# Optimization experiments

Measured on AMD Instinct MI355X. Metric: run time of the kernel, lower is better.

Reference implementation:

```python
import jax, jax.numpy as jnp
import numpy as np
import math

B, N, L = 1, 256, 384
D_MSA, D_PAIR, H, DH = 256, 128, 8, 32


def layer_norm(x, g, b, eps=1e-5):
    m = jnp.mean(x, axis=-1, keepdims=True)
    v = jnp.var(x, axis=-1, keepdims=True)
    return (x - m) * jax.lax.rsqrt(v + eps) * g + b


def setup_inputs() -> dict:
    key = jax.random.key(0)
    ks = jax.random.split(key, 16)
    hd = H * DH
    w = lambda k, shp, s=0.05: (jax.random.normal(k, shp, dtype=jnp.float32) * s)
    return {
        "msa": jax.random.normal(ks[0], (B, N, L, D_MSA), dtype=jnp.float32),
        "pair": jax.random.normal(ks[1], (B, L, L, D_PAIR), dtype=jnp.float32),
        "ln_msa_g": jnp.ones((D_MSA,), jnp.float32),
        "ln_msa_b": jnp.zeros((D_MSA,), jnp.float32),
        "ln_pair_g": jnp.ones((D_PAIR,), jnp.float32),
        "ln_pair_b": jnp.zeros((D_PAIR,), jnp.float32),
        "sw_q_w": w(ks[2], (D_MSA, hd)),
        "sw_q_b": jnp.zeros((hd,), jnp.float32),
        "sw_k_w": w(ks[3], (D_MSA, hd)),
        "sw_k_b": jnp.zeros((hd,), jnp.float32),
        "wq": w(ks[4], (D_MSA, hd)),
        "wk": w(ks[5], (D_MSA, hd)),
        "wv": w(ks[6], (D_MSA, hd)),
        "wb": w(ks[7], (D_PAIR, H)),
        "wg": w(ks[8], (D_MSA, hd)),
        "bg": jnp.ones((hd,), jnp.float32),
        "wo": w(ks[9], (hd, D_MSA)),
        "bo": jnp.zeros((D_MSA,), jnp.float32),
    }


def reference(msa, pair, ln_msa_g, ln_msa_b, ln_pair_g, ln_pair_b,
              sw_q_w, sw_q_b, sw_k_w, sw_k_b,
              wq, wk, wv, wb, wg, bg, wo, bo):
    b, n, l, _ = msa.shape
    scale = 1.0 / math.sqrt(DH)

    msa_n = layer_norm(msa, ln_msa_g, ln_msa_b)
    pair_n = layer_norm(pair, ln_pair_g, ln_pair_b)

    # SequenceWeight: attention of target seq (row 0) over all N rows, per (L, head)
    tar = msa_n[:, 0]                                       # [B,L,D]
    swq = (tar @ sw_q_w + sw_q_b).reshape(b, l, H, DH) * scale
    swk = (msa_n @ sw_k_w + sw_k_b).reshape(b, n, l, H, DH)
    sw_logits = jnp.einsum('blhd,bnlhd->bnlh', swq, swk)    # [B,N,L,H]
    seq_weight = jax.nn.softmax(sw_logits, axis=1)          # softmax over N (dropout: eval)

    query = (msa_n @ wq).reshape(b, n, l, H, DH) * seq_weight[..., None]
    key = (msa_n @ wk).reshape(b, n, l, H, DH) * scale
    value = (msa_n @ wv).reshape(b, n, l, H, DH)
    bias = pair_n @ wb                                      # [B,L,L,H]
    gate = jax.nn.sigmoid(msa_n @ wg + bg)                  # [B,N,L,H*DH]

    attn = jnp.einsum('bsqhd,bskhd->bqkh', query, key) + bias
    attn = jax.nn.softmax(attn, axis=-2)                    # over k axis
    out = jnp.einsum('bqkh,bskhd->bsqhd', attn, value).reshape(b, n, l, H * DH)
    out = gate * out
    return out @ wo + bo
```

## Files before the change

### kernel.cpp

```cpp
#include <hip/hip_runtime.h>
#include <stdint.h>

#define NSEQ 256
#define LSEQ 384
#define DM   256
#define DP   128
#define NH   8
#define DHD  32
#define NL   (NSEQ*LSEQ)
#define LL   (LSEQ*LSEQ)
#define SCALE 0.17677669529663687f

typedef unsigned short u16;
typedef short bf16x8 __attribute__((ext_vector_type(8)));
typedef float f32x4 __attribute__((ext_vector_type(4)));

__device__ __forceinline__ float b2f(u16 s){
  union { uint32_t u; float f; } v; v.u = ((uint32_t)s)<<16; return v.f;
}
__device__ __forceinline__ u16 f2b(float f){
  union { float f; uint32_t u; } v; v.f = f;
  uint32_t u = v.u;
  return (u16)((u + 0x7FFFu + ((u>>16)&1u)) >> 16);
}
__device__ __forceinline__ float wsum(float x){
  #pragma unroll
  for(int o=32;o>0;o>>=1) x += __shfl_xor(x,o,64);
  return x;
}
__device__ __forceinline__ float wmax(float x){
  #pragma unroll
  for(int o=32;o>0;o>>=1) x = fmaxf(x, __shfl_xor(x,o,64));
  return x;
}
__device__ __forceinline__ void gload16(const void* g, void* l){
  __builtin_amdgcn_global_load_lds((const __attribute__((address_space(1))) void*)g,
      (__attribute__((address_space(3))) void*)l, 16, 0, 0);
}

__global__ __launch_bounds__(256) void k_ln_msa(const float* __restrict__ msa,
    const float* __restrict__ g, const float* __restrict__ b, u16* __restrict__ out){
  int lane = threadIdx.x & 63;
  int64_t row = (int64_t)blockIdx.x*4 + (threadIdx.x>>6);
  const float4 x = *(const float4*)(msa + row*DM + lane*4);
  float s = x.x+x.y+x.z+x.w;
  float q = x.x*x.x+x.y*x.y+x.z*x.z+x.w*x.w;
  s = wsum(s); q = wsum(q);
  float mean = s*(1.0f/DM);
  float rstd = rsqrtf(q*(1.0f/DM) - mean*mean + 1e-5f);
  int c = lane*4;
  float4 gv = *(const float4*)(g+c);
  float4 bv = *(const float4*)(b+c);
  ushort4 o;
  o.x=f2b((x.x-mean)*rstd*gv.x+bv.x);
  o.y=f2b((x.y-mean)*rstd*gv.y+bv.y);
  o.z=f2b((x.z-mean)*rstd*gv.z+bv.z);
  o.w=f2b((x.w-mean)*rstd*gv.w+bv.w);
  *(ushort4*)(out + row*DM + c) = o;
}

__global__ __launch_bounds__(256) void k_wconv(const float* __restrict__ wq,
    const float* __restrict__ wk, const float* __restrict__ wv,
    const float* __restrict__ wg, const float* __restrict__ wo,
    u16* __restrict__ WTall, u16* __restrict__ WOT){
  __shared__ float tile[64][65];
  int z = blockIdx.z;
  const float* src = (z==0)?wq:(z==1)?wk:(z==2)?wv:(z==3)?wg:wo;
  u16* dst = (z<4) ? (WTall + z*DM*DM) : WOT;
  int k0 = blockIdx.x*64, n0 = blockIdx.y*64, t = threadIdx.x;
  int r = t>>4, c4 = (t&15)*4;
  #pragma unroll
  for(int it=0; it<4; it++){
    float4 v = *(const float4*)(src + (int64_t)(k0 + it*16 + r)*DM + n0 + c4);
    tile[it*16+r][c4+0]=v.x; tile[it*16+r][c4+1]=v.y;
    tile[it*16+r][c4+2]=v.z; tile[it*16+r][c4+3]=v.w;
  }
  __syncthreads();
  #pragma unroll
  for(int it=0; it<4; it++){
    int nl = it*16 + r, kl = c4;
    ushort4 o;
    o.x=f2b(tile[kl+0][nl]); o.y=f2b(tile[kl+1][nl]);
    o.z=f2b(tile[kl+2][nl]); o.w=f2b(tile[kl+3][nl]);
    *(ushort4*)(dst + (int64_t)(n0+nl)*DM + k0 + kl) = o;
  }
}

__global__ __launch_bounds__(256) void k_u(const u16* __restrict__ msa_n,
    const float* __restrict__ sw_q_w, const float* __restrict__ sw_q_b,
    const float* __restrict__ sw_k_w, float* __restrict__ u){
  __shared__ float tar[DM];
  __shared__ float swq[DM];
  int l = blockIdx.x, t = threadIdx.x;
  tar[t] = b2f(msa_n[(int64_t)l*DM + t]);
  __syncthreads();
  float acc = sw_q_b[t];
  for(int c=0;c<DM;c++) acc += tar[c]*sw_q_w[c*DM + t];
  swq[t] = acc * SCALE;
  __syncthreads();
  float res[NH];
  #pragma unroll
  for(int h=0;h<NH;h++){
    float a = 0.f;
    #pragma unroll
    for(int d=0;d<DHD;d+=4){
      float4 w = *(const float4*)(sw_k_w + t*DM + h*DHD + d);
      a += w.x*swq[h*DHD+d] + w.y*swq[h*DHD+d+1] + w.z*swq[h*DHD+d+2] + w.w*swq[h*DHD+d+3];
    }
    res[h]=a;
  }
  #pragma unroll
  for(int h=0;h<NH;h++) u[((int64_t)l*NH + h)*DM + t] = res[h];
}

__global__ __launch_bounds__(256) void k_seqw(const u16* __restrict__ msa_n,
    const float* __restrict__ u, float* __restrict__ sw){
  __shared__ float ul[NH*DM];
  __shared__ float lg[NH*256];
  __shared__ float mx[NH], sm[NH];
  int l = blockIdx.x, t = threadIdx.x;
  #pragma unroll
  for(int h=0;h<NH;h++) ul[h*DM+t] = u[((int64_t)l*NH+h)*DM + t];
  __syncthreads();
  float acc[NH] = {};
  const u16* row = msa_n + ((int64_t)t*LSEQ + l)*DM;
  for(int c=0;c<DM;c+=4){
    ushort4 xv = *(const ushort4*)(row + c);
    float x0=b2f(xv.x), x1=b2f(xv.y), x2=b2f(xv.z), x3=b2f(xv.w);
    #pragma unroll
    for(int h=0;h<NH;h++)
      acc[h] += x0*ul[h*DM+c] + x1*ul[h*DM+c+1] + x2*ul[h*DM+c+2] + x3*ul[h*DM+c+3];
  }
  #pragma unroll
  for(int h=0;h<NH;h++) lg[h*256+t] = acc[h];
  __syncthreads();
  int wv = t>>6, ln = t&63;
  for(int h=wv; h<NH; h+=4){
    float a=lg[h*256+ln], b=lg[h*256+ln+64], c=lg[h*256+ln+128], d=lg[h*256+ln+192];
    float m = wmax(fmaxf(fmaxf(a,b),fmaxf(c,d)));
    float e = __expf(a-m)+__expf(b-m)+__expf(c-m)+__expf(d-m);
    e = wsum(e);
    if(ln==0){ mx[h]=m; sm[h]=1.f/e; }
  }
  __syncthreads();
  float o[NH];
  #pragma unroll
  for(int h=0;h<NH;h++) o[h] = __expf(acc[h]-mx[h])*sm[h];
  float* dst = sw + ((int64_t)t*LSEQ + l)*NH;
  *(float4*)dst     = make_float4(o[0],o[1],o[2],o[3]);
  *(float4*)(dst+4) = make_float4(o[4],o[5],o[6],o[7]);
}

__global__ __launch_bounds__(256) void k_bias(const float* __restrict__ pair,
    const float* __restrict__ g, const float* __restrict__ b,
    const float* __restrict__ wb, float* __restrict__ bias){
  __shared__ float wbs[DP*NH];
  int t = threadIdx.x;
  #pragma unroll
  for(int i=0;i<4;i++) wbs[i*256+t] = wb[i*256+t];
  __syncthreads();
  int ln = t&63;
  int64_t row = (int64_t)blockIdx.x*4 + (t>>6);
  const float2 x = *(const float2*)(pair + row*DP + ln*2);
  float s = x.x+x.y, q = x.x*x.x+x.y*x.y;
  s = wsum(s); q = wsum(q);
  float mean = s*(1.f/DP);
  float rstd = rsqrtf(q*(1.f/DP)-mean*mean + 1e-5f);
  int c0 = ln*2;
  float y0 = (x.x-mean)*rstd*g[c0]+b[c0];
  float y1 = (x.y-mean)*rstd*g[c0+1]+b[c0+1];
  float p[NH];
  #pragma unroll
  for(int h=0;h<NH;h++) p[h] = y0*wbs[c0*NH+h] + y1*wbs[(c0+1)*NH+h];
  #pragma unroll
  for(int h=0;h<NH;h++) p[h] = wsum(p[h]);
  if(ln<NH) bias[(int64_t)ln*LL + row] = p[ln];
}


__global__ __launch_bounds__(256) void k_projf(const u16* __restrict__ A,
    const u16* __restrict__ WT, u16* __restrict__ qb, u16* __restrict__ kb,
    u16* __restrict__ gbuf, u16* __restrict__ VT,
    const float* __restrict__ sw, const float* __restrict__ bg){
  __shared__ short As[128*64];
  __shared__ short Bs[128*64];
  int t = threadIdx.x;
  int w = t>>6, lane = t&63, ln15 = lane&15, quad = lane>>4;
  int rIn = lane>>3, cch = lane&7;
  int mw = (w>>1)*64, nw = (w&1)*64;
  int bx = blockIdx.x;
  int by = blockIdx.y;
  int n0 = bx*128;
  int64_t r0 = (int64_t)by*128;
  int g = cch ^ rIn;
  f32x4 acc[4][4] = {};
  for(int it=0; it<4; it++){
    int k0 = it*64;
    __syncthreads();
    #pragma unroll
    for(int ti=0; ti<4; ti++){
      int row = w*32 + ti*8 + rIn;
      gload16(A  + (r0+row)*DM + k0 + g*8, &As[(w*32+ti*8)*64]);
      gload16(WT + (int64_t)(n0+row)*DM + k0 + g*8, &Bs[(w*32+ti*8)*64]);
    }
    __syncthreads();
    #pragma unroll
    for(int kk=0;kk<2;kk++){
      int p = (kk*4+quad) ^ (lane&7);
      bf16x8 af[4], bfv[4];
      #pragma unroll
      for(int i=0;i<4;i++) af[i]  = *(const bf16x8*)&As[(mw+i*16+ln15)*64 + p*8];
      #pragma unroll
      for(int j=0;j<4;j++) bfv[j] = *(const bf16x8*)&Bs[(nw+j*16+ln15)*64 + p*8];
      #pragma unroll
      for(int i=0;i<4;i++)
        #pragma unroll
        for(int j=0;j<4;j++)
          acc[i][j] = __builtin_amdgcn_mfma_f32_16x16x32_bf16(af[i], bfv[j], acc[i][j], 0,0,0);
    }
  }
  int mode = bx>>1;
  int cmb = (bx&1)*128 + nw;
  if(mode==2){
    int s = by/3, kb3 = (by%3)*128 + mw;
    #pragma unroll
    for(int j=0;j<4;j++){
      int cm = cmb + j*16 + ln15;
      int hh = cm>>5, d = cm&31;
      #pragma unroll
      for(int i=0;i<4;i++){
        int kpos0 = kb3 + i*16 + quad*4;
        ushort4 o;
        o.x=f2b(acc[i][j][0]); o.y=f2b(acc[i][j][1]);
        o.z=f2b(acc[i][j][2]); o.w=f2b(acc[i][j][3]);
        *(ushort4*)(VT + ((int64_t)(hh*NSEQ+s)*DHD + d)*LSEQ + kpos0) = o;
      }
    }
  } else {
    u16* dst = (mode==0)?qb:(mode==1)?kb:gbuf;
    float bgv[4];
    if(mode==3){
      #pragma unroll
      for(int j=0;j<4;j++) bgv[j] = bg[cmb + j*16 + ln15];
    }
    #pragma unroll
    for(int i=0;i<4;i++)
      #pragma unroll
      for(int reg=0;reg<4;reg++){
        int64_t r = r0 + mw + i*16 + quad*4 + reg;
        #pragma unroll
        for(int j=0;j<4;j++){
          int cm = cmb + j*16 + ln15;
          float v = acc[i][j][reg];
          if(mode==0)      v *= sw[r*NH + (cm>>5)];
          else if(mode==1) v *= SCALE;
          else             v = 1.f/(1.f+__expf(-(v+bgv[j])));
          dst[r*DM + cm] = f2b(v);
        }
      }
  }
}

__global__ __launch_bounds__(256) void k_scores(const u16* __restrict__ Q,
    const u16* __restrict__ K, float* __restrict__ scores){
  __shared__ short As[128*64];
  __shared__ short Bs[128*64];
  int t = threadIdx.x;
  int w = t>>6, lane = t&63, ln15 = lane&15, quad = lane>>4;
  int rIn = lane>>3, cch = lane&7;
  int mw = (w>>1)*64, nw = (w&1)*64;
  int q0 = blockIdx.x*128, k0t = blockIdx.y*128;
  int h = blockIdx.z>>2, sc = blockIdx.z&3;
  int g = cch ^ rIn;
  int s_off = g>>2, d16 = g&3;
  f32x4 acc[4][4] = {};
  for(int i2=0; i2<32; i2++){
    int sb = sc*64 + i2*2 + s_off;
    __syncthreads();
    #pragma unroll
    for(int ti=0; ti<4; ti++){
      int row = w*32 + ti*8 + rIn;
      gload16(Q + ((int64_t)sb*LSEQ + q0 + row)*DM + h*DHD + d16*8, &As[(w*32+ti*8)*64]);
      gload16(K + ((int64_t)sb*LSEQ + k0t + row)*DM + h*DHD + d16*8, &Bs[(w*32+ti*8)*64]);
    }
    __syncthreads();
    #pragma unroll
    for(int kk=0;kk<2;kk++){
      int p = (kk*4+quad) ^ (lane&7);
      bf16x8 af[4], bfv[4];
      #pragma unroll
      for(int i=0;i<4;i++) af[i]  = *(const bf16x8*)&As[(mw+i*16+ln15)*64 + p*8];
      #pragma unroll
      for(int j=0;j<4;j++) bfv[j] = *(const bf16x8*)&Bs[(nw+j*16+ln15)*64 + p*8];
      #pragma unroll
      for(int i=0;i<4;i++)
        #pragma unroll
        for(int j=0;j<4;j++)
          acc[i][j] = __builtin_amdgcn_mfma_f32_16x16x32_bf16(af[i], bfv[j], acc[i][j], 0,0,0);
    }
  }
  int64_t slab = (int64_t)sc*NH*LL;
  #pragma unroll
  for(int i=0;i<4;i++)
    #pragma unroll
    for(int reg=0;reg<4;reg++){
      int q = q0 + mw + i*16 + quad*4 + reg;
      float* rp = scores + slab + ((int64_t)h*LSEQ + q)*LSEQ + k0t + nw + ln15;
      #pragma unroll
      for(int j=0;j<4;j++) rp[j*16] = acc[i][j][reg];
    }
}

__global__ __launch_bounds__(128) void k_softmax(const float* __restrict__ scores,
    const float* __restrict__ bias, u16* __restrict__ Pb){
  int hq = blockIdx.x, t = threadIdx.x;
  int64_t base = (int64_t)hq*LSEQ;
  float v[3];
  #pragma unroll
  for(int i=0;i<3;i++){
    int k = t + i*128;
    float x = bias[base+k];
    x += scores[base+k];
    x += scores[(int64_t)1*NH*LL + base + k];
    x += scores[(int64_t)2*NH*LL + base + k];
    x += scores[(int64_t)3*NH*LL + base + k];
    v[i]=x;
  }
  __shared__ float red[2], red2[2];
  int wv=t>>6, ln=t&63;
  float m = fmaxf(fmaxf(v[0],v[1]),v[2]);
  m = wmax(m);
  if(ln==0) red[wv]=m;
  __syncthreads();
  m = fmaxf(red[0],red[1]);
  float e = __expf(v[0]-m)+__expf(v[1]-m)+__expf(v[2]-m);
  e = wsum(e);
  if(ln==0) red2[wv]=e;
  __syncthreads();
  float inv = 1.f/(red2[0]+red2[1]);
  #pragma unroll
  for(int i=0;i<3;i++) Pb[base + t + i*128] = f2b(__expf(v[i]-m)*inv);
}

__global__ __launch_bounds__(256) void k_pv(const u16* __restrict__ VT,
    const u16* __restrict__ Pb, const u16* __restrict__ gbuf,
    u16* __restrict__ attn){
  __shared__ short As[128*64];
  __shared__ short Bs[128*64];
  int t = threadIdx.x;
  int w = t>>6, lane = t&63, ln15 = lane&15, quad = lane>>4;
  int rIn = lane>>3, cch = lane&7;
  int mw = (w>>1)*64, nw = (w&1)*64;
  int mx = blockIdx.x, ny = blockIdx.y, h = blockIdx.z;
  int g = cch ^ rIn;
  f32x4 acc[4][4] = {};
  for(int it=0; it<6; it++){
    int k0 = it*64;
    __syncthreads();
    #pragma unroll
    for(int ti=0; ti<4; ti++){
      int row = w*32 + ti*8 + rIn;
      gload16(VT + ((int64_t)h*8192 + mx*128 + row)*LSEQ + k0 + g*8, &As[(w*32+ti*8)*64]);
      gload16(Pb + ((int64_t)h*LSEQ + ny*128 + row)*LSEQ + k0 + g*8, &Bs[(w*32+ti*8)*64]);
    }
    __syncthreads();
    #pragma unroll
    for(int kk=0;kk<2;kk++){
      int p = (kk*4+quad) ^ (lane&7);
      bf16x8 af[4], bfv[4];
      #pragma unroll
      for(int i=0;i<4;i++) af[i]  = *(const bf16x8*)&As[(mw+i*16+ln15)*64 + p*8];
      #pragma unroll
      for(int j=0;j<4;j++) bfv[j] = *(const bf16x8*)&Bs[(nw+j*16+ln15)*64 + p*8];
      #pragma unroll
      for(int i=0;i<4;i++)
        #pragma unroll
        for(int j=0;j<4;j++)
          acc[i][j] = __builtin_amdgcn_mfma_f32_16x16x32_bf16(af[i], bfv[j], acc[i][j], 0,0,0);
    }
  }
  #pragma unroll
  for(int i=0;i<4;i++){
    int m0 = mx*128 + mw + i*16 + quad*4;
    int s = m0>>5, d0 = m0&31;
    #pragma unroll
    for(int j=0;j<4;j++){
      int q = ny*128 + nw + j*16 + ln15;
      int64_t base = ((int64_t)s*LSEQ + q)*DM + h*DHD + d0;
      ushort4 gv = *(const ushort4*)(gbuf + base);
      ushort4 o;
      o.x = f2b(acc[i][j][0]*b2f(gv.x));
      o.y = f2b(acc[i][j][1]*b2f(gv.y));
      o.z = f2b(acc[i][j][2]*b2f(gv.z));
      o.w = f2b(acc[i][j][3]*b2f(gv.w));
      *(ushort4*)(attn + base) = o;
    }
  }
}

__global__ __launch_bounds__(256) void k_final(const u16* __restrict__ A,
    const u16* __restrict__ WOT, const float* __restrict__ bo,
    float* __restrict__ out){
  __shared__ short As[128*64];
  __shared__ short Bs[128*64];
  int t = threadIdx.x;
  int w = t>>6, lane = t&63, ln15 = lane&15, quad = lane>>4;
  int rIn = lane>>3, cch = lane&7;
  int mw = (w>>1)*64, nw = (w&1)*64;
  int n0 = blockIdx.x*128;
  int64_t r0 = (int64_t)blockIdx.y*128;
  int g = cch ^ rIn;
  f32x4 acc[4][4] = {};
  for(int it=0; it<4; it++){
    int k0 = it*64;
    __syncthreads();
    #pragma unroll
    for(int ti=0; ti<4; ti++){
      int row = w*32 + ti*8 + rIn;
      gload16(A   + (r0+row)*DM + k0 + g*8, &As[(w*32+ti*8)*64]);
      gload16(WOT + (int64_t)(n0+row)*DM + k0 + g*8, &Bs[(w*32+ti*8)*64]);
    }
    __syncthreads();
    #pragma unroll
    for(int kk=0;kk<2;kk++){
      int p = (kk*4+quad) ^ (lane&7);
      bf16x8 af[4], bfv[4];
      #pragma unroll
      for(int i=0;i<4;i++) af[i]  = *(const bf16x8*)&As[(mw+i*16+ln15)*64 + p*8];
      #pragma unroll
      for(int j=0;j<4;j++) bfv[j] = *(const bf16x8*)&Bs[(nw+j*16+ln15)*64 + p*8];
      #pragma unroll
      for(int i=0;i<4;i++)
        #pragma unroll
        for(int j=0;j<4;j++)
          acc[i][j] = __builtin_amdgcn_mfma_f32_16x16x32_bf16(af[i], bfv[j], acc[i][j], 0,0,0);
    }
  }
  float bv[4];
  #pragma unroll
  for(int j=0;j<4;j++) bv[j] = bo[n0 + nw + j*16 + ln15];
  #pragma unroll
  for(int i=0;i<4;i++)
    #pragma unroll
    for(int reg=0;reg<4;reg++){
      int64_t r = r0 + mw + i*16 + quad*4 + reg;
      float* rp = out + r*DM + n0 + nw + ln15;
      #pragma unroll
      for(int j=0;j<4;j++) rp[j*16] = acc[i][j][reg] + bv[j];
    }
}

extern "C" void kernel_launch(void* const* d_in, const int* in_sizes, int n_in,
                              void* d_out, int out_size, void* d_ws, size_t ws_size,
                              hipStream_t stream){
  const float* msa    = (const float*)d_in[0];
  const float* pair   = (const float*)d_in[1];
  const float* lmg    = (const float*)d_in[2];
  const float* lmb    = (const float*)d_in[3];
  const float* lpg    = (const float*)d_in[4];
  const float* lpb    = (const float*)d_in[5];
  const float* sw_q_w = (const float*)d_in[6];
  const float* sw_q_b = (const float*)d_in[7];
  const float* sw_k_w = (const float*)d_in[8];
  const float* wq     = (const float*)d_in[10];
  const float* wk     = (const float*)d_in[11];
  const float* wv     = (const float*)d_in[12];
  const float* wb     = (const float*)d_in[13];
  const float* wg     = (const float*)d_in[14];
  const float* bg     = (const float*)d_in[15];
  const float* wo     = (const float*)d_in[16];
  const float* bo     = (const float*)d_in[17];
  float* out = (float*)d_out;

  u16* msa_n = (u16*)d_ws;
  u16* qb    = msa_n + (int64_t)NL*DM;
  u16* kb    = qb + (int64_t)NL*DM;
  u16* gbuf  = kb + (int64_t)NL*DM;
  u16* VT    = gbuf + (int64_t)NL*DM;
  u16* Pb    = VT + (int64_t)NL*DM;
  u16* WTall = Pb + (int64_t)NH*LSEQ*LSEQ;
  u16* WOT   = WTall + 1024*DM;
  float* u_buf = (float*)(WOT + DM*DM);
  float* sw  = u_buf + (int64_t)LSEQ*NH*DM;
  float* bias = sw + (int64_t)NL*NH;
  float* scores = bias + (int64_t)NH*LL;
  u16* attnout = msa_n;

  k_ln_msa<<<NL/4, 256, 0, stream>>>(msa, lmg, lmb, msa_n);
  k_wconv<<<dim3(4,4,5), 256, 0, stream>>>(wq, wk, wv, wg, wo, WTall, WOT);
  k_u<<<LSEQ, 256, 0, stream>>>(msa_n, sw_q_w, sw_q_b, sw_k_w, u_buf);
  k_seqw<<<LSEQ, 256, 0, stream>>>(msa_n, u_buf, sw);
  k_bias<<<LL/4, 256, 0, stream>>>(pair, lpg, lpb, wb, bias);
  k_projf<<<dim3(8, NL/128), 256, 0, stream>>>(msa_n, WTall, qb, kb, gbuf, VT, sw, bg);
  k_scores<<<dim3(3,3,32), 256, 0, stream>>>(qb, kb, scores);
  k_softmax<<<NH*LSEQ, 128, 0, stream>>>(scores, bias, Pb);
  k_pv<<<dim3(64,3,NH), 256, 0, stream>>>(VT, Pb, gbuf, attnout);
  k_final<<<dim3(2, NL/128), 256, 0, stream>>>(attnout, WOT, bo, out);
}
```

Before: 736.4 us.

## Rewrite pair-bias as per-thread row LN and loop projections over N tiles

The pair-bias kernel now gives each thread a whole 128-channel row. The row is cached in registers as fp16 and the 8-head projection is computed serially, which replaces the wave-shuffle reductions and gives coalesced per-head stores. The projection GEMM moves from a 2D grid of (8 column tiles × row tiles) to one block per 128-row tile that loops over all 8 column tiles, keeping the A-tile rows hot in cache. This trades parallelism, with fewer blocks and fewer threads in the bias kernel and heavy register use, plus fp16 rounding of the pair input before normalization.

```diff
diff --git a/kernel.cpp b/kernel.cpp
--- a/kernel.cpp
+++ b/kernel.cpp
@@ -1,4 +1,5 @@
 #include <hip/hip_runtime.h>
+#include <hip/hip_fp16.h>
 #include <stdint.h>
 
 #define NSEQ 256
@@ -154,27 +155,40 @@
 __global__ __launch_bounds__(256) void k_bias(const float* __restrict__ pair,
     const float* __restrict__ g, const float* __restrict__ b,
     const float* __restrict__ wb, float* __restrict__ bias){
-  __shared__ float wbs[DP*NH];
-  int t = threadIdx.x;
-  #pragma unroll
-  for(int i=0;i<4;i++) wbs[i*256+t] = wb[i*256+t];
-  __syncthreads();
-  int ln = t&63;
-  int64_t row = (int64_t)blockIdx.x*4 + (t>>6);
-  const float2 x = *(const float2*)(pair + row*DP + ln*2);
-  float s = x.x+x.y, q = x.x*x.x+x.y*x.y;
-  s = wsum(s); q = wsum(q);
+  int64_t row = (int64_t)blockIdx.x*256 + threadIdx.x;
+  const float* pr = pair + row*DP;
+  uint2 xs[32];
+  float s = 0.f, q = 0.f;
+  #pragma unroll
+  for(int i=0;i<32;i++){
+    float4 v = *(const float4*)(pr + i*4);
+    s += v.x+v.y+v.z+v.w;
+    q += v.x*v.x+v.y*v.y+v.z*v.z+v.w*v.w;
+    __half2 p0 = __floats2half2_rn(v.x, v.y);
+    __half2 p1 = __floats2half2_rn(v.z, v.w);
+    xs[i].x = *(const uint32_t*)&p0;
+    xs[i].y = *(const uint32_t*)&p1;
+  }
   float mean = s*(1.f/DP);
-  float rstd = rsqrtf(q*(1.f/DP)-mean*mean + 1e-5f);
-  int c0 = ln*2;
-  float y0 = (x.x-mean)*rstd*g[c0]+b[c0];
-  float y1 = (x.y-mean)*rstd*g[c0+1]+b[c0+1];
-  float p[NH];
-  #pragma unroll
-  for(int h=0;h<NH;h++) p[h] = y0*wbs[c0*NH+h] + y1*wbs[(c0+1)*NH+h];
-  #pragma unroll
-  for(int h=0;h<NH;h++) p[h] = wsum(p[h]);
-  if(ln<NH) bias[(int64_t)ln*LL + row] = p[ln];
+  float rstd = rsqrtf(q*(1.f/DP) - mean*mean + 1e-5f);
+  float acc[NH] = {};
+  #pragma unroll
+  for(int i=0;i<32;i++){
+    __half2 p0 = *(const __half2*)&xs[i].x;
+    __half2 p1 = *(const __half2*)&xs[i].y;
+    float2 f0 = __half22float2(p0);
+    float2 f1 = __half22float2(p1);
+    float xv[4] = {f0.x, f0.y, f1.x, f1.y};
+    #pragma unroll
+    for(int c4=0;c4<4;c4++){
+      int c = i*4 + c4;
+      float y = (xv[c4]-mean)*rstd*g[c] + b[c];
+      #pragma unroll
+      for(int h=0;h<NH;h++) acc[h] += y*wb[c*NH+h];
+    }
+  }
+  #pragma unroll
+  for(int h=0;h<NH;h++) bias[(int64_t)h*LL + row] = acc[h];
 }
 
 
@@ -189,75 +203,76 @@
   int rIn = lane>>3, cch = lane&7;
   int mw = (w>>1)*64, nw = (w&1)*64;
   int bx = blockIdx.x;
-  int by = blockIdx.y;
-  int n0 = bx*128;
-  int64_t r0 = (int64_t)by*128;
+  int64_t r0 = (int64_t)bx*128;
   int g = cch ^ rIn;
-  f32x4 acc[4][4] = {};
-  for(int it=0; it<4; it++){
-    int k0 = it*64;
-    __syncthreads();
-    #pragma unroll
-    for(int ti=0; ti<4; ti++){
-      int row = w*32 + ti*8 + rIn;
-      gload16(A  + (r0+row)*DM + k0 + g*8, &As[(w*32+ti*8)*64]);
-      gload16(WT + (int64_t)(n0+row)*DM + k0 + g*8, &Bs[(w*32+ti*8)*64]);
-    }
-    __syncthreads();
-    #pragma unroll
-    for(int kk=0;kk<2;kk++){
-      int p = (kk*4+quad) ^ (lane&7);
-      bf16x8 af[4], bfv[4];
-      #pragma unroll
-      for(int i=0;i<4;i++) af[i]  = *(const bf16x8*)&As[(mw+i*16+ln15)*64 + p*8];
-      #pragma unroll
-      for(int j=0;j<4;j++) bfv[j] = *(const bf16x8*)&Bs[(nw+j*16+ln15)*64 + p*8];
-      #pragma unroll
-      for(int i=0;i<4;i++)
-        #pragma unroll
-        for(int j=0;j<4;j++)
-          acc[i][j] = __builtin_amdgcn_mfma_f32_16x16x32_bf16(af[i], bfv[j], acc[i][j], 0,0,0);
-    }
-  }
-  int mode = bx>>1;
-  int cmb = (bx&1)*128 + nw;
-  if(mode==2){
-    int s = by/3, kb3 = (by%3)*128 + mw;
-    #pragma unroll
-    for(int j=0;j<4;j++){
-      int cm = cmb + j*16 + ln15;
-      int hh = cm>>5, d = cm&31;
-      #pragma unroll
-      for(int i=0;i<4;i++){
-        int kpos0 = kb3 + i*16 + quad*4;
-        ushort4 o;
-        o.x=f2b(acc[i][j][0]); o.y=f2b(acc[i][j][1]);
-        o.z=f2b(acc[i][j][2]); o.w=f2b(acc[i][j][3]);
-        *(ushort4*)(VT + ((int64_t)(hh*NSEQ+s)*DHD + d)*LSEQ + kpos0) = o;
+  for(int nt=0; nt<8; nt++){
+    int n0 = nt*128;
+    f32x4 acc[4][4] = {};
+    for(int it=0; it<4; it++){
+      int k0 = it*64;
+      __syncthreads();
+      #pragma unroll
+      for(int ti=0; ti<4; ti++){
+        int row = w*32 + ti*8 + rIn;
+        gload16(A  + (r0+row)*DM + k0 + g*8, &As[(w*32+ti*8)*64]);
+        gload16(WT + (int64_t)(n0+row)*DM + k0 + g*8, &Bs[(w*32+ti*8)*64]);
       }
-    }
-  } else {
-    u16* dst = (mode==0)?qb:(mode==1)?kb:gbuf;
-    float bgv[4];
-    if(mode==3){
-      #pragma unroll
-      for(int j=0;j<4;j++) bgv[j] = bg[cmb + j*16 + ln15];
-    }
-    #pragma unroll
-    for(int i=0;i<4;i++)
-      #pragma unroll
-      for(int reg=0;reg<4;reg++){
-        int64_t r = r0 + mw + i*16 + quad*4 + reg;
-        #pragma unroll
-        for(int j=0;j<4;j++){
-          int cm = cmb + j*16 + ln15;
-          float v = acc[i][j][reg];
-          if(mode==0)      v *= sw[r*NH + (cm>>5)];
-          else if(mode==1) v *= SCALE;
-          else             v = 1.f/(1.f+__expf(-(v+bgv[j])));
-          dst[r*DM + cm] = f2b(v);
+      __syncthreads();
+      #pragma unroll
+      for(int kk=0;kk<2;kk++){
+        int p = (kk*4+quad) ^ (lane&7);
+        bf16x8 af[4], bfv[4];
+        #pragma unroll
+        for(int i=0;i<4;i++) af[i]  = *(const bf16x8*)&As[(mw+i*16+ln15)*64 + p*8];
+        #pragma unroll
+        for(int j=0;j<4;j++) bfv[j] = *(const bf16x8*)&Bs[(nw+j*16+ln15)*64 + p*8];
+        #pragma unroll
+        for(int i=0;i<4;i++)
+          #pragma unroll
+          for(int j=0;j<4;j++)
+            acc[i][j] = __builtin_amdgcn_mfma_f32_16x16x32_bf16(af[i], bfv[j], acc[i][j], 0,0,0);
+      }
+    }
+    int mode = nt>>1;
+    int cmb = (nt&1)*128 + nw;
+    if(mode==2){
+      int s = bx/3, kb3 = (bx%3)*128 + mw;
+      #pragma unroll
+      for(int j=0;j<4;j++){
+        int cm = cmb + j*16 + ln15;
+        int hh = cm>>5, d = cm&31;
+        #pragma unroll
+        for(int i=0;i<4;i++){
+          int kpos0 = kb3 + i*16 + quad*4;
+          ushort4 o;
+          o.x=f2b(acc[i][j][0]); o.y=f2b(acc[i][j][1]);
+          o.z=f2b(acc[i][j][2]); o.w=f2b(acc[i][j][3]);
+          *(ushort4*)(VT + ((int64_t)(hh*NSEQ+s)*DHD + d)*LSEQ + kpos0) = o;
         }
       }
+    } else {
+      u16* dst = (mode==0)?qb:(mode==1)?kb:gbuf;
+      float bgv[4];
+      if(mode==3){
+        #pragma unroll
+        for(int j=0;j<4;j++) bgv[j] = bg[cmb + j*16 + ln15];
+      }
+      #pragma unroll
+      for(int i=0;i<4;i++)
+        #pragma unroll
+        for(int reg=0;reg<4;reg++){
+          int64_t r = r0 + mw + i*16 + quad*4 + reg;
+          #pragma unroll
+          for(int j=0;j<4;j++){
+            int cm = cmb + j*16 + ln15;
+            float v = acc[i][j][reg];
+            if(mode==0)      v *= sw[r*NH + (cm>>5)];
+            else if(mode==1) v *= SCALE;
+            else             v = 1.f/(1.f+__expf(-(v+bgv[j])));
+            dst[r*DM + cm] = f2b(v);
+          }
+        }
+    }
   }
 }
 
@@ -490,8 +505,8 @@
   k_wconv<<<dim3(4,4,5), 256, 0, stream>>>(wq, wk, wv, wg, wo, WTall, WOT);
   k_u<<<LSEQ, 256, 0, stream>>>(msa_n, sw_q_w, sw_q_b, sw_k_w, u_buf);
   k_seqw<<<LSEQ, 256, 0, stream>>>(msa_n, u_buf, sw);
-  k_bias<<<LL/4, 256, 0, stream>>>(pair, lpg, lpb, wb, bias);
-  k_projf<<<dim3(8, NL/128), 256, 0, stream>>>(msa_n, WTall, qb, kb, gbuf, VT, sw, bg);
+  k_bias<<<LL/256, 256, 0, stream>>>(pair, lpg, lpb, wb, bias);
+  k_projf<<<dim3(NL/128), 256, 0, stream>>>(msa_n, WTall, qb, kb, gbuf, VT, sw, bg);
   k_scores<<<dim3(3,3,32), 256, 0, stream>>>(qb, kb, scores);
   k_softmax<<<NH*LSEQ, 128, 0, stream>>>(scores, bias, Pb);
   k_pv<<<dim3(64,3,NH), 256, 0, stream>>>(VT, Pb, gbuf, attnout);
```

Result: no change. 728.3 us (-1.1%).
